# Optimization experiments

Hardware: AMD Instinct MI355X
Metric: run time of the kernel (lower is better)

The kernel has to match this reference:

```python
import jax, jax.numpy as jnp
import numpy as np

B, T, D_MODEL, HEAD_DIM = 8, 2048, 1024, 128


def setup_inputs() -> dict:
    key = jax.random.key(0)
    k1, k2, k3, k4 = jax.random.split(key, 4)
    scale = 1.0 / np.sqrt(D_MODEL)
    return {
        "x": jax.random.normal(k1, (B, T, D_MODEL), dtype=jnp.float32),
        "Wq": jax.random.normal(k2, (HEAD_DIM, D_MODEL), dtype=jnp.float32) * scale,
        "Wk": jax.random.normal(k3, (HEAD_DIM, D_MODEL), dtype=jnp.float32) * scale,
        "Wv": jax.random.normal(k4, (HEAD_DIM, D_MODEL), dtype=jnp.float32) * scale,
    }


def reference(x, Wq, Wk, Wv) -> jnp.ndarray:
    # x: [B, T, C]; torch Linear(no bias): y = x @ W.T, W: [head_dim, d_model]
    q = jnp.einsum("btc,hc->bth", x, Wq)  # [B, T, H]
    k = jnp.einsum("btc,hc->bth", x, Wk)
    v = jnp.einsum("btc,hc->bth", x, Wv)
    head_dim = Wq.shape[0]
    scores = jnp.einsum("bqh,bkh->bqk", q, k) / jnp.sqrt(jnp.float32(head_dim))  # [B, T, T]
    T_ = x.shape[1]
    causal = jnp.tril(jnp.ones((T_, T_), dtype=bool))
    scores = jnp.where(causal, scores, -jnp.inf)
    probs = jax.nn.softmax(scores, axis=-1)
    # dropout is identity at inference (eval mode)
    out = jnp.einsum("bqk,bkh->bqh", probs, v)  # [B, T, head_dim]
    return out
```

## Files before the change

kernel.cpp:

```cpp
#include <hip/hip_runtime.h>
#include <hip/hip_bf16.h>
#include <math.h>

#define T_ 2048
#define C_ 1024
#define H_ 128
#define NB 8
#define WN 131072
#define SC 0.08838834764831845f

typedef __attribute__((ext_vector_type(8))) short bf16x8;
typedef __attribute__((ext_vector_type(8))) unsigned short u16x8;
typedef __attribute__((ext_vector_type(4))) float f32x4;

#define MFMA16(a,b,c) __builtin_amdgcn_mfma_f32_16x16x32_bf16((a),(b),(c),0,0,0)

__device__ __forceinline__ unsigned short f2bf(float f) {
    union { float f; unsigned u; } v; v.f = f;
    unsigned r = v.u + 0x7fffu + ((v.u >> 16) & 1u);
    return (unsigned short)(r >> 16);
}
__device__ __forceinline__ float bf2f(unsigned short u) {
    union { unsigned u; float f; } v; v.u = ((unsigned)u) << 16; return v.f;
}
__device__ __forceinline__ unsigned pk2bf(float a, float b) {
    __hip_bfloat162 h = __float22bfloat162_rn(float2{a, b});
    union { __hip_bfloat162 h; unsigned u; } v; v.h = h; return v.u;
}
__device__ __forceinline__ void gld16(void* lds, const void* g) {
    __builtin_amdgcn_global_load_lds(
        (const __attribute__((address_space(1))) unsigned*)g,
        (__attribute__((address_space(3))) unsigned*)lds, 16, 0, 0);
}

__global__ __launch_bounds__(256) void wconv(const float* __restrict__ Wq,
                                             const float* __restrict__ Wk,
                                             const float* __restrict__ Wv,
                                             unsigned short* __restrict__ Wb) {
    int e = (blockIdx.x * 256 + threadIdx.x) * 8;
    int which = e >> 17;
    int off = e & (WN - 1);
    const float* src = (which == 0) ? Wq : (which == 1 ? Wk : Wv);
    float s = (which == 0) ? SC : 1.0f;
    const float4* p = (const float4*)(src + off);
    float4 a = p[0], b = p[1];
    uint4 o = { pk2bf(a.x * s, a.y * s), pk2bf(a.z * s, a.w * s),
                pk2bf(b.x * s, b.y * s), pk2bf(b.z * s, b.w * s) };
    *(uint4*)(Wb + e) = o;
}

__global__ __launch_bounds__(256, 2) void proj(const float* __restrict__ x,
                                               const unsigned short* __restrict__ Wb,
                                               unsigned short* __restrict__ Q,
                                               unsigned short* __restrict__ K,
                                               unsigned short* __restrict__ V) {
    __shared__ unsigned short Xs[2][64][64];
    __shared__ unsigned short Ws[2][192][64];

    const int tid  = threadIdx.x;
    const int wave = tid >> 6, lane = tid & 63;
    const int quad = lane >> 4, l16 = lane & 15;
    const int wm   = wave >> 1, wn = wave & 1;
    const int m0   = (blockIdx.x >> 1) * 64;
    const int n0   = (blockIdx.x & 1) * 192;

    f32x4 acc[2][6];
    #pragma unroll
    for (int i = 0; i < 2; i++)
        #pragma unroll
        for (int j = 0; j < 6; j++) acc[i][j] = {0.f, 0.f, 0.f, 0.f};

    const int xrow = tid >> 2, xcg = tid & 3;
    const float* xg = x + (size_t)(m0 + xrow) * C_ + xcg * 16;
    const int xk = xrow & 7;
    const unsigned short* wg = Wb + (size_t)(n0 + wave * 48 + (lane >> 3)) * C_
                               + (size_t)(((lane & 7) ^ (lane >> 3)) * 8);

    float4 xr0, xr1, xr2, xr3;
    #define ISSUE(buf, kc) do {                                                   \
        _Pragma("unroll")                                                         \
        for (int i = 0; i < 6; i++)                                               \
            gld16(&Ws[buf][wave * 48 + i * 8][0], wg + (size_t)i * 8 * C_ + (kc));\
        const float* xp = xg + (kc);                                              \
        xr0 = *(const float4*)xp;        xr1 = *(const float4*)(xp + 4);          \
        xr2 = *(const float4*)(xp + 8);  xr3 = *(const float4*)(xp + 12);         \
    } while (0)

    #define XWRITE(buf) do {                                                      \
        uint4 u0 = { pk2bf(xr0.x, xr0.y), pk2bf(xr0.z, xr0.w),                    \
                     pk2bf(xr1.x, xr1.y), pk2bf(xr1.z, xr1.w) };                  \
        uint4 u1 = { pk2bf(xr2.x, xr2.y), pk2bf(xr2.z, xr2.w),                    \
                     pk2bf(xr3.x, xr3.y), pk2bf(xr3.z, xr3.w) };                  \
        *(uint4*)&Xs[buf][xrow][((2 * xcg)     ^ xk) * 8] = u0;                   \
        *(uint4*)&Xs[buf][xrow][((2 * xcg + 1) ^ xk) * 8] = u1;                   \
    } while (0)

    ISSUE(0, 0);
    XWRITE(0);
    for (int it = 0; it < 16; it++) {
        __syncthreads();
        const int buf = it & 1;
        if (it < 15) ISSUE(buf ^ 1, (it + 1) * 64);
        const int key = l16 & 7;
        bf16x8 af[2][2];
        #pragma unroll
        for (int kk = 0; kk < 2; kk++)
            #pragma unroll
            for (int mf = 0; mf < 2; mf++)
                af[mf][kk] = *(bf16x8*)&Xs[buf][wm * 32 + mf * 16 + l16]
                                          [((kk * 4 + quad) ^ key) * 8];
        #pragma unroll
        for (int kk = 0; kk < 2; kk++)
            #pragma unroll
            for (int nf = 0; nf < 6; nf++) {
                bf16x8 bq = *(bf16x8*)&Ws[buf][wn * 96 + nf * 16 + l16]
                                         [((kk * 4 + quad) ^ key) * 8];
                acc[0][nf] = MFMA16(af[0][kk], bq, acc[0][nf]);
                acc[1][nf] = MFMA16(af[1][kk], bq, acc[1][nf]);
            }
        if (it < 15) XWRITE(buf ^ 1);
    }
    #undef ISSUE
    #undef XWRITE

    #pragma unroll
    for (int nf = 0; nf < 6; nf++) {
        int nb = n0 + wn * 96 + nf * 16;
        int which = nb >> 7;
        unsigned short* dst = (which == 0) ? Q : (which == 1 ? K : V);
        int c = (nb & 127) + l16;
        #pragma unroll
        for (int mf = 0; mf < 2; mf++)
            #pragma unroll
            for (int r = 0; r < 4; r++)
                dst[(size_t)(m0 + wm * 32 + mf * 16 + quad * 4 + r) * H_ + c] = f2bf(acc[mf][nf][r]);
    }
}

__global__ __launch_bounds__(256, 2) void attn(const unsigned short* __restrict__ Qg,
                                               const unsigned short* __restrict__ Kg,
                                               const unsigned short* __restrict__ Vg,
                                               unsigned short* __restrict__ Ob,
                                               float* __restrict__ Ml) {
    const int bx = blockIdx.x;
    const int s  = bx & 7, qt = 31 - (bx >> 3);
    const int b  = blockIdx.y;
    const int qbase = qt * 64, kstart = s * 256;
    if (kstart > qbase) return;
    const int kend  = (kstart + 256 < qbase + 64) ? kstart + 256 : qbase + 64;
    const int niter = (kend - kstart) >> 6;

    __shared__ unsigned short Ks[2][4][64][32];
    __shared__ unsigned short Vt[2][128 * 64];
    __shared__ unsigned short Ps[4][16][64];

    const int tid = threadIdx.x, wave = tid >> 6, lane = tid & 63;
    const int quad = lane >> 4, l16 = lane & 15;
    const size_t base = (size_t)b * T_ * H_;

    const unsigned short* ksrc = Kg + base + (size_t)(kstart + (lane >> 2)) * H_ + wave * 32 + (lane & 3) * 8;
    #pragma unroll
    for (int p = 0; p < 4; p++) gld16(&Ks[0][wave][p * 16][0], ksrc + (size_t)p * 16 * H_);
    const unsigned short* vsrc = Vg + base + (size_t)(kstart + wave * 8 + quad * 2) * H_ + l16 * 8;
    u16x8 vr[2][2];
    vr[0][0] = *(const u16x8*)vsrc;             vr[0][1] = *(const u16x8*)(vsrc + H_);
    vr[1][0] = *(const u16x8*)(vsrc + 32 * H_); vr[1][1] = *(const u16x8*)(vsrc + 33 * H_);

    bf16x8 qf[4];
    const unsigned short* qp = Qg + base + (size_t)(qbase + wave * 16 + l16) * H_ + quad * 8;
    #pragma unroll
    for (int kk = 0; kk < 4; kk++) qf[kk] = *(const bf16x8*)(qp + kk * 32);

    f32x4 o[8];
    #pragma unroll
    for (int i = 0; i < 8; i++) o[i] = {0.f, 0.f, 0.f, 0.f};
    float m_i = -INFINITY, l_i = 0.f;
    const int swz = (l16 & 7) << 3;
    const int qg = qbase + wave * 16 + l16;

    #define VTWRITE(bufi) do {                                                       \
        _Pragma("unroll")                                                            \
        for (int g = 0; g < 2; g++) {                                                \
            int t0 = wave * 8 + g * 32 + quad * 2;                                   \
            int t8 = t0 >> 3;                                                        \
            _Pragma("unroll")                                                        \
            for (int j = 0; j < 8; j++) {                                            \
                int h = l16 * 8 + j;                                                 \
                unsigned pk = (unsigned)(unsigned short)vr[g][0][j]                  \
                            | ((unsigned)(unsigned short)vr[g][1][j] << 16);         \
                int blk = (t8 ^ (h & 7) ^ ((h >> 3) & 7)) & 7;                       \
                *(unsigned*)&Vt[bufi][h * 64 + blk * 8 + (t0 & 7)] = pk;             \
            }                                                                        \
        }                                                                            \
    } while (0)

    VTWRITE(0);
    __syncthreads();

    for (int kt = 0; ; kt++) {
        const int kbase = kstart + kt * 64;
        const int buf = kt & 1;
        const bool more = (kt + 1 < niter);
        if (more) {
            ksrc += 64 * H_;
            #pragma unroll
            for (int p = 0; p < 4; p++) gld16(&Ks[buf ^ 1][wave][p * 16][0], ksrc + (size_t)p * 16 * H_);
            vsrc += 64 * H_;
            vr[0][0] = *(const u16x8*)vsrc;             vr[0][1] = *(const u16x8*)(vsrc + H_);
            vr[1][0] = *(const u16x8*)(vsrc + 32 * H_); vr[1][1] = *(const u16x8*)(vsrc + 33 * H_);
        }
        f32x4 st[4];
        #pragma unroll
        for (int nf = 0; nf < 4; nf++) st[nf] = {0.f, 0.f, 0.f, 0.f};
        __builtin_amdgcn_s_setprio(1);
        #pragma unroll
        for (int kk = 0; kk < 4; kk++)
            #pragma unroll
            for (int nf = 0; nf < 4; nf++) {
                bf16x8 kfr = *(bf16x8*)&Ks[buf][kk][nf * 16 + l16][quad * 8];
                st[nf] = MFMA16(kfr, qf[kk], st[nf]);
            }
        __builtin_amdgcn_s_setprio(0);
        if (kbase + 64 > qbase) {
            #pragma unroll
            for (int nf = 0; nf < 4; nf++) {
                int kg = kbase + nf * 16 + quad * 4;
                #pragma unroll
                for (int r = 0; r < 4; r++)
                    if (kg + r > qg) st[nf][r] = -INFINITY;
            }
        }
        float mx = st[0][0];
        #pragma unroll
        for (int nf = 0; nf < 4; nf++)
            #pragma unroll
            for (int r = 0; r < 4; r++) mx = fmaxf(mx, st[nf][r]);
        mx = fmaxf(mx, __shfl_xor(mx, 16, 64));
        mx = fmaxf(mx, __shfl_xor(mx, 32, 64));
        float mnew = fmaxf(m_i, mx);
        float al = __expf(m_i - mnew);
        m_i = mnew;
        float rs = 0.f;
        #pragma unroll
        for (int nf = 0; nf < 4; nf++)
            #pragma unroll
            for (int r = 0; r < 4; r++) {
                float e = __expf(st[nf][r] - mnew);
                st[nf][r] = e; rs += e;
            }
        rs += __shfl_xor(rs, 16, 64);
        rs += __shfl_xor(rs, 32, 64);
        l_i = al * l_i + rs;
        #pragma unroll
        for (int nf = 0; nf < 4; nf++) {
            uint2 pk = { pk2bf(st[nf][0], st[nf][1]), pk2bf(st[nf][2], st[nf][3]) };
            *(uint2*)&Ps[wave][l16][(nf * 16 + quad * 4) ^ swz] = pk;
        }
        float a0 = __shfl(al, quad * 4 + 0, 64), a1 = __shfl(al, quad * 4 + 1, 64);
        float a2 = __shfl(al, quad * 4 + 2, 64), a3 = __shfl(al, quad * 4 + 3, 64);
        #pragma unroll
        for (int i = 0; i < 8; i++) {
            o[i][0] *= a0; o[i][1] *= a1; o[i][2] *= a2; o[i][3] *= a3;
        }
        bf16x8 pa0 = *(bf16x8*)&Ps[wave][l16][(quad * 8) ^ swz];
        bf16x8 pa1 = *(bf16x8*)&Ps[wave][l16][(32 + quad * 8) ^ swz];
        __builtin_amdgcn_s_setprio(1);
        #pragma unroll
        for (int nf = 0; nf < 8; nf++) {
            int h = nf * 16 + l16;
            int ex = (h & 7) ^ ((h >> 3) & 7);
            bf16x8 v0 = *(bf16x8*)&Vt[buf][h * 64 + ((quad ^ ex) & 7) * 8];
            bf16x8 v1 = *(bf16x8*)&Vt[buf][h * 64 + (((quad + 4) ^ ex) & 7) * 8];
            o[nf] = MFMA16(pa0, v0, o[nf]);
            o[nf] = MFMA16(pa1, v1, o[nf]);
        }
        __builtin_amdgcn_s_setprio(0);
        if (!more) break;
        VTWRITE(buf ^ 1);
        __syncthreads();
    }
    #undef VTWRITE

    const int g2 = qt >> 2;
    const int Pq = 2 * g2 * (g2 + 1) + (qt & 3) * (g2 + 1);
    const int slot = (Pq + s) * NB + b;
    float lq[4];
    #pragma unroll
    for (int r = 0; r < 4; r++) lq[r] = __shfl(l_i, quad * 4 + r, 64);
    const size_t obase = (size_t)slot * 64 * 128;
    #pragma unroll
    for (int r = 0; r < 4; r++) {
        float invl = 1.0f / lq[r];
        #pragma unroll
        for (int nf = 0; nf < 8; nf++)
            Ob[obase + (size_t)(wave * 16 + quad * 4 + r) * 128 + nf * 16 + l16] = f2bf(o[nf][r] * invl);
    }
    if (lane < 16) {
        int ridx = slot * 64 + wave * 16 + l16;
        Ml[ridx * 2]     = m_i;
        Ml[ridx * 2 + 1] = l_i;
    }
}

__global__ __launch_bounds__(256) void merge(const unsigned short* __restrict__ Ob,
                                             const float* __restrict__ Ml,
                                             float* __restrict__ out) {
    const int qt = blockIdx.x, b = blockIdx.y;
    const int g = qt >> 2;
    const int Pq = 2 * g * (g + 1) + (qt & 3) * (g + 1);
    const int ns = g + 1;
    const int tid = threadIdx.x;
    const int row = tid >> 2, c0 = (tid & 3) * 32;

    float mv[8], lv[8], mg = -INFINITY;
    for (int s2 = 0; s2 < ns; s2++) {
        int slot = (Pq + s2) * NB + b;
        mv[s2] = Ml[(slot * 64 + row) * 2];
        lv[s2] = Ml[(slot * 64 + row) * 2 + 1];
        mg = fmaxf(mg, mv[s2]);
    }
    float L = 0.f, w[8];
    for (int s2 = 0; s2 < ns; s2++) { w[s2] = lv[s2] * __expf(mv[s2] - mg); L += w[s2]; }
    float inv = 1.0f / L;

    float accv[32];
    #pragma unroll
    for (int i = 0; i < 32; i++) accv[i] = 0.f;
    for (int s2 = 0; s2 < ns; s2++) {
        int slot = (Pq + s2) * NB + b;
        const unsigned short* op = Ob + ((size_t)(slot * 64 + row)) * 128 + c0;
        #pragma unroll
        for (int cc = 0; cc < 4; cc++) {
            u16x8 v = *(const u16x8*)(op + cc * 8);
            #pragma unroll
            for (int j = 0; j < 8; j++) accv[cc * 8 + j] += w[s2] * bf2f(v[j]);
        }
    }
    float* od = out + ((size_t)(b * T_ + qt * 64 + row)) * 128 + c0;
    #pragma unroll
    for (int cc = 0; cc < 8; cc++) {
        float4 w4 = { accv[cc*4] * inv, accv[cc*4+1] * inv, accv[cc*4+2] * inv, accv[cc*4+3] * inv };
        *(float4*)(od + cc * 4) = w4;
    }
}

extern "C" void kernel_launch(void* const* d_in, const int* in_sizes, int n_in,
                              void* d_out, int out_size, void* d_ws, size_t ws_size,
                              hipStream_t stream) {
    const float* x  = (const float*)d_in[0];
    const float* Wq = (const float*)d_in[1];
    const float* Wk = (const float*)d_in[2];
    const float* Wv = (const float*)d_in[3];

    char* ws = (char*)d_ws;
    unsigned short* Wb = (unsigned short*)ws;
    unsigned short* Q  = (unsigned short*)(ws + (size_t) 1 * (1u << 20));
    unsigned short* K  = (unsigned short*)(ws + (size_t) 5 * (1u << 20));
    unsigned short* V  = (unsigned short*)(ws + (size_t) 9 * (1u << 20));
    unsigned short* Ob = (unsigned short*)(ws + (size_t)13 * (1u << 20));
    float*          Ml = (float*)(ws + (size_t)32 * (1u << 20));
    float* out = (float*)d_out;

    hipLaunchKernelGGL(wconv, dim3(192), dim3(256), 0, stream, Wq, Wk, Wv, Wb);
    hipLaunchKernelGGL(proj,  dim3(512), dim3(256), 0, stream, x, Wb, Q, K, V);
    hipLaunchKernelGGL(attn,  dim3(256, NB), dim3(256), 0, stream, Q, K, V, Ob, Ml);
    hipLaunchKernelGGL(merge, dim3(32, NB), dim3(256), 0, stream, Ob, Ml, out);
}
```

Measured before the change: 182.7 us.

## Drop split-K attention and merge kernel; one block per query tile

```diff
diff --git a/kernel.cpp b/kernel.cpp
--- a/kernel.cpp
+++ b/kernel.cpp
@@ -137,18 +137,14 @@
     }
 }
 
-__global__ __launch_bounds__(256, 2) void attn(const unsigned short* __restrict__ Qg,
+__global__ __launch_bounds__(256, 1) void attn(const unsigned short* __restrict__ Qg,
                                                const unsigned short* __restrict__ Kg,
                                                const unsigned short* __restrict__ Vg,
-                                               unsigned short* __restrict__ Ob,
-                                               float* __restrict__ Ml) {
-    const int bx = blockIdx.x;
-    const int s  = bx & 7, qt = 31 - (bx >> 3);
+                                               float* __restrict__ out) {
+    const int qt = blockIdx.x;
     const int b  = blockIdx.y;
-    const int qbase = qt * 64, kstart = s * 256;
-    if (kstart > qbase) return;
-    const int kend  = (kstart + 256 < qbase + 64) ? kstart + 256 : qbase + 64;
-    const int niter = (kend - kstart) >> 6;
+    const int qbase = qt * 64;
+    const int niter = qt + 1;
 
     __shared__ unsigned short Ks[2][4][64][32];
     __shared__ unsigned short Vt[2][128 * 64];
@@ -158,10 +154,10 @@
     const int quad = lane >> 4, l16 = lane & 15;
     const size_t base = (size_t)b * T_ * H_;
 
-    const unsigned short* ksrc = Kg + base + (size_t)(kstart + (lane >> 2)) * H_ + wave * 32 + (lane & 3) * 8;
+    const unsigned short* ksrc = Kg + base + (size_t)(lane >> 2) * H_ + wave * 32 + (lane & 3) * 8;
     #pragma unroll
     for (int p = 0; p < 4; p++) gld16(&Ks[0][wave][p * 16][0], ksrc + (size_t)p * 16 * H_);
-    const unsigned short* vsrc = Vg + base + (size_t)(kstart + wave * 8 + quad * 2) * H_ + l16 * 8;
+    const unsigned short* vsrc = Vg + base + (size_t)(wave * 8 + quad * 2) * H_ + l16 * 8;
     u16x8 vr[2][2];
     vr[0][0] = *(const u16x8*)vsrc;             vr[0][1] = *(const u16x8*)(vsrc + H_);
     vr[1][0] = *(const u16x8*)(vsrc + 32 * H_); vr[1][1] = *(const u16x8*)(vsrc + 33 * H_);
@@ -198,7 +194,7 @@
     __syncthreads();
 
     for (int kt = 0; ; kt++) {
-        const int kbase = kstart + kt * 64;
+        const int kbase = kt * 64;
         const int buf = kt & 1;
         const bool more = (kt + 1 < niter);
         if (more) {
@@ -281,66 +277,16 @@
     }
     #undef VTWRITE
 
-    const int g2 = qt >> 2;
-    const int Pq = 2 * g2 * (g2 + 1) + (qt & 3) * (g2 + 1);
-    const int slot = (Pq + s) * NB + b;
     float lq[4];
     #pragma unroll
     for (int r = 0; r < 4; r++) lq[r] = __shfl(l_i, quad * 4 + r, 64);
-    const size_t obase = (size_t)slot * 64 * 128;
     #pragma unroll
     for (int r = 0; r < 4; r++) {
         float invl = 1.0f / lq[r];
+        float* od = out + (size_t)(b * T_ + qbase + wave * 16 + quad * 4 + r) * H_ + l16;
         #pragma unroll
         for (int nf = 0; nf < 8; nf++)
-            Ob[obase + (size_t)(wave * 16 + quad * 4 + r) * 128 + nf * 16 + l16] = f2bf(o[nf][r] * invl);
-    }
-    if (lane < 16) {
-        int ridx = slot * 64 + wave * 16 + l16;
-        Ml[ridx * 2]     = m_i;
-        Ml[ridx * 2 + 1] = l_i;
-    }
-}
-
-__global__ __launch_bounds__(256) void merge(const unsigned short* __restrict__ Ob,
-                                             const float* __restrict__ Ml,
-                                             float* __restrict__ out) {
-    const int qt = blockIdx.x, b = blockIdx.y;
-    const int g = qt >> 2;
-    const int Pq = 2 * g * (g + 1) + (qt & 3) * (g + 1);
-    const int ns = g + 1;
-    const int tid = threadIdx.x;
-    const int row = tid >> 2, c0 = (tid & 3) * 32;
-
-    float mv[8], lv[8], mg = -INFINITY;
-    for (int s2 = 0; s2 < ns; s2++) {
-        int slot = (Pq + s2) * NB + b;
-        mv[s2] = Ml[(slot * 64 + row) * 2];
-        lv[s2] = Ml[(slot * 64 + row) * 2 + 1];
-        mg = fmaxf(mg, mv[s2]);
-    }
-    float L = 0.f, w[8];
-    for (int s2 = 0; s2 < ns; s2++) { w[s2] = lv[s2] * __expf(mv[s2] - mg); L += w[s2]; }
-    float inv = 1.0f / L;
-
-    float accv[32];
-    #pragma unroll
-    for (int i = 0; i < 32; i++) accv[i] = 0.f;
-    for (int s2 = 0; s2 < ns; s2++) {
-        int slot = (Pq + s2) * NB + b;
-        const unsigned short* op = Ob + ((size_t)(slot * 64 + row)) * 128 + c0;
-        #pragma unroll
-        for (int cc = 0; cc < 4; cc++) {
-            u16x8 v = *(const u16x8*)(op + cc * 8);
-            #pragma unroll
-            for (int j = 0; j < 8; j++) accv[cc * 8 + j] += w[s2] * bf2f(v[j]);
-        }
-    }
-    float* od = out + ((size_t)(b * T_ + qt * 64 + row)) * 128 + c0;
-    #pragma unroll
-    for (int cc = 0; cc < 8; cc++) {
-        float4 w4 = { accv[cc*4] * inv, accv[cc*4+1] * inv, accv[cc*4+2] * inv, accv[cc*4+3] * inv };
-        *(float4*)(od + cc * 4) = w4;
+            od[nf * 16] = o[nf][r] * invl;
     }
 }
 
@@ -357,12 +303,9 @@
     unsigned short* Q  = (unsigned short*)(ws + (size_t) 1 * (1u << 20));
     unsigned short* K  = (unsigned short*)(ws + (size_t) 5 * (1u << 20));
     unsigned short* V  = (unsigned short*)(ws + (size_t) 9 * (1u << 20));
-    unsigned short* Ob = (unsigned short*)(ws + (size_t)13 * (1u << 20));
-    float*          Ml = (float*)(ws + (size_t)32 * (1u << 20));
     float* out = (float*)d_out;
 
     hipLaunchKernelGGL(wconv, dim3(192), dim3(256), 0, stream, Wq, Wk, Wv, Wb);
     hipLaunchKernelGGL(proj,  dim3(512), dim3(256), 0, stream, x, Wb, Q, K, V);
-    hipLaunchKernelGGL(attn,  dim3(256, NB), dim3(256), 0, stream, Q, K, V, Ob, Ml);
-    hipLaunchKernelGGL(merge, dim3(32, NB), dim3(256), 0, stream, Ob, Ml, out);
-}
+    hipLaunchKernelGGL(attn,  dim3(32, NB), dim3(256), 0, stream, Q, K, V, out);
+}
```

Result: no change. 185.4 us (+1.5%).
